# Kernel optimization log

Hardware: AMD Instinct MI355X
Metric: run time of the kernel (lower is better)

Reference implementation:

```python
import jax, jax.numpy as jnp
import numpy as np

B, N, K = 32, 2048, 16          # graphs, nodes per graph, knn neighbors
F_IN, F_OUT, P = 32, 64, 3      # feature dims, pos dim


def setup_inputs() -> dict:
    key = jax.random.key(0)
    ks = jax.random.split(key, 6)
    x = jax.random.normal(ks[0], (B * N, F_IN), dtype=jnp.float32)
    pos = jax.random.normal(ks[1], (B * N, P), dtype=jnp.float32)
    # contiguous equal-size graphs: batch[i] = i // N
    batch = (jnp.arange(B * N, dtype=jnp.int32) // N).astype(jnp.int32)
    W_edge = jax.random.normal(ks[2], (2 * F_IN, F_OUT), dtype=jnp.float32) * 0.1
    b_edge = jax.random.normal(ks[3], (F_OUT,), dtype=jnp.float32) * 0.1
    W_nn = jax.random.normal(ks[4], (F_IN, F_OUT), dtype=jnp.float32) * 0.1
    b_nn = jax.random.normal(ks[5], (F_OUT,), dtype=jnp.float32) * 0.1
    return {"x": x, "pos": pos, "W_edge": W_edge, "b_edge": b_edge,
            "W_nn": W_nn, "b_nn": b_nn, "batch": batch}


def reference(x, pos, W_edge, b_edge, W_nn, b_nn, batch):
    # batch is contiguous with N nodes per graph -> reshape to [B, N, .]
    xb = x.reshape(B, N, F_IN)
    pb = pos.reshape(B, N, P)

    # --- knn_graph on pos, per graph (flow='source_to_target') ---
    sq = jnp.sum(pb * pb, axis=-1)                                   # [B, N]
    d2 = sq[:, :, None] + sq[:, None, :] - 2.0 * jnp.einsum('bnd,bmd->bnm', pb, pb)
    d2 = d2 + jnp.eye(N, dtype=d2.dtype) * 1e30                      # exclude self-loops
    _, idx = jax.lax.top_k(-d2, K)                                   # idx[b, i, k] = k-th nearest j of i

    # --- EdgeConv: message = edge_nn(concat(x_i, x_j - x_i)), aggr=max at i ---
    x_j = jnp.take_along_axis(xb, idx.reshape(B, N * K, 1), axis=1).reshape(B, N, K, F_IN)
    x_i = xb[:, :, None, :]                                          # [B, N, 1, F_IN]
    msg = jnp.concatenate([jnp.broadcast_to(x_i, (B, N, K, F_IN)), x_j - x_i], axis=-1)
    h = jax.nn.relu(msg @ W_edge + b_edge)                           # [B, N, K, F_OUT]
    edge_out = jnp.max(h, axis=2)                                    # max-aggregate over neighbors

    # --- skip branch: nn(x) ---
    skip = jax.nn.relu(xb @ W_nn + b_nn)                             # [B, N, F_OUT]

    return (edge_out + skip).reshape(B * N, F_OUT)
```

## Files before the change

kernel.cpp:

```cpp
#include <hip/hip_runtime.h>

#define NB     32
#define NPTS   2048
#define KNN    16
#define FIN    32
#define FOUT   64

typedef __attribute__((ext_vector_type(8))) short bf16x8;
typedef __attribute__((ext_vector_type(4))) float f32x4;

__device__ inline unsigned bf16pk(float lo, float hi) {
    unsigned a = __float_as_uint(lo), b = __float_as_uint(hi);
    a = (a + 0x7fffu + ((a >> 16) & 1u)) >> 16;
    b = (b + 0x7fffu + ((b >> 16) & 1u)) >> 16;
    return (a & 0xffffu) | (b << 16);
}


#define CEA(x, y) { float _t = fminf(x, y); y = fmaxf(x, y); x = _t; }
#define CED(x, y) { float _t = fmaxf(x, y); y = fminf(x, y); x = _t; }

#define BMERGE16(dk) \
    CEA(dk[0],dk[8])  CEA(dk[1],dk[9])  CEA(dk[2],dk[10]) CEA(dk[3],dk[11]) \
    CEA(dk[4],dk[12]) CEA(dk[5],dk[13]) CEA(dk[6],dk[14]) CEA(dk[7],dk[15]) \
    CEA(dk[0],dk[4])  CEA(dk[1],dk[5])  CEA(dk[2],dk[6])  CEA(dk[3],dk[7])  \
    CEA(dk[8],dk[12]) CEA(dk[9],dk[13]) CEA(dk[10],dk[14]) CEA(dk[11],dk[15]) \
    CEA(dk[0],dk[2])  CEA(dk[1],dk[3])  CEA(dk[4],dk[6])  CEA(dk[5],dk[7])  \
    CEA(dk[8],dk[10]) CEA(dk[9],dk[11]) CEA(dk[12],dk[14]) CEA(dk[13],dk[15]) \
    CEA(dk[0],dk[1])  CEA(dk[2],dk[3])  CEA(dk[4],dk[5])  CEA(dk[6],dk[7])  \
    CEA(dk[8],dk[9])  CEA(dk[10],dk[11]) CEA(dk[12],dk[13]) CEA(dk[14],dk[15])

#define NET8(a) \
    CED(a[0],a[1]) CED(a[2],a[3]) CED(a[4],a[5]) CED(a[6],a[7]) \
    CED(a[0],a[2]) CED(a[1],a[3]) CED(a[4],a[6]) CED(a[5],a[7]) \
    CED(a[1],a[2]) CED(a[5],a[6]) \
    CED(a[0],a[4]) CED(a[1],a[5]) CED(a[2],a[6]) CED(a[3],a[7]) \
    CED(a[2],a[4]) CED(a[3],a[5]) \
    CED(a[1],a[2]) CED(a[3],a[4]) CED(a[5],a[6])

__global__ __launch_bounds__(256) void sq_kernel(
    const float* __restrict__ pos, float4* __restrict__ P4)
{
    const int i = blockIdx.x * 256 + threadIdx.x;
    const float px = pos[i*3 + 0];
    const float py = pos[i*3 + 1];
    const float pz = pos[i*3 + 2];
    const float sq = __fadd_rn(__fadd_rn(__fmul_rn(px,px), __fmul_rn(py,py)),
                               __fmul_rn(pz,pz));
    P4[i] = make_float4(px, py, pz, sq);
}

#define CH   8
#define CHL  (NPTS / CH)

#define D2P(C, DST)                                                        \
    {                                                                      \
        float _dot = __fmaf_rn(me.z, (C).z,                                \
                      __fmaf_rn(me.y, (C).y, __fmul_rn(me.x, (C).x)));     \
        DST = __fmaf_rn(-2.0f, _dot, (C).w);                               \
    }

#define SBATCH2(JB, EXCLF)                                                 \
    {                                                                      \
        float a[8], a2[8];                                                 \
        _Pragma("unroll")                                                  \
        for (int i = 0; i < 8; ++i) {                                      \
            const int j = (JB) + i;                                        \
            const float4 c = pb4[j];                                       \
            float d2;                                                      \
            D2P(c, d2)                                                     \
            a[i] = (EXCLF && j == q) ? 1e30f : d2;                         \
        }                                                                  \
        _Pragma("unroll")                                                  \
        for (int i = 0; i < 8; ++i) {                                      \
            const int j = (JB) + 8 + i;                                    \
            const float4 c = pb4[j];                                       \
            float d2;                                                      \
            D2P(c, d2)                                                     \
            a2[i] = (EXCLF && j == q) ? 1e30f : d2;                        \
        }                                                                  \
        NET8(a)                                                            \
        NET8(a2)                                                           \
        _Pragma("unroll")                                                  \
        for (int i = 0; i < 8; ++i) dk[8+i] = fminf(dk[8+i], a[i]);        \
        BMERGE16(dk)                                                       \
        _Pragma("unroll")                                                  \
        for (int i = 0; i < 8; ++i) dk[8+i] = fminf(dk[8+i], a2[i]);       \
        BMERGE16(dk)                                                       \
    }

#define APP(DD, JJ)                                                        \
    if ((DD) <= tthr) {                                                    \
        if ((DD) < tthr) {                                                 \
            if (cntS + cntT >= KNN) --cntT;                                \
            JL[base + cntS * 64 + l] = (JJ);                               \
            ++cntS;                                                        \
        } else if (cntS + cntT < KNN) {                                    \
            JL[base + (KNN - 1 - cntT) * 64 + l] = (JJ);                   \
            ++cntT;                                                        \
        }                                                                  \
    }

#define RESC(JJ, EXCLF)                                                    \
    {                                                                      \
        const float4 c = pb4[(JJ)];                                        \
        float d2;                                                          \
        D2P(c, d2)                                                         \
        if (EXCLF && (JJ) == q) d2 = 1e30f;                                \
        APP(d2, (JJ))                                                      \
    }

#define ESTRIDE 66

__global__ __launch_bounds__(512, 8) void knn_mlp_kernel(
    const float4* __restrict__ P4, const float* __restrict__ x,
    const float* __restrict__ W_edge, const float* __restrict__ b_edge,
    const float* __restrict__ W_nn,   const float* __restrict__ b_nn,
    float* __restrict__ out)
{
    __shared__ __attribute__((aligned(16))) char smem[38912];
    float* V    = (float*)smem;
    int*   CNTS = (int*)(smem + 32768);
    int*   IDX  = (int*)(smem + 34816);

    const int b    = blockIdx.x >> 5;
    const int slab = blockIdx.x & 31;
    const int t    = threadIdx.x;
    const int w    = __builtin_amdgcn_readfirstlane(t >> 6);
    const int l    = t & 63;

    {
        const float4* __restrict__ pb4 = P4 + (size_t)b * NPTS;

        const int    q  = slab * 64 + l;
        const float4 me = pb4[q];

        float dk[KNN];
        #pragma unroll
        for (int s = 0; s < KNN; ++s) dk[s] = 1e30f;

        const int j0  = w * CHL;
        const int exw = slab >> 2;
        const int lo  = j0 + (slab & 3) * 64;

        if (w == exw) {
            for (int jb = j0;      jb < lo;        jb += 16) SBATCH2(jb, false)
            for (int jb = lo;      jb < lo + 64;   jb += 16) SBATCH2(jb, true)
            for (int jb = lo + 64; jb < j0 + CHL;  jb += 16) SBATCH2(jb, false)
        } else {
            for (int jb = j0;      jb < j0 + CHL;  jb += 16) SBATCH2(jb, false)
        }

        #pragma unroll
        for (int s = 0; s < KNN; ++s)
            V[(w * KNN + s) * 64 + l] = dk[s];
        __syncthreads();

        for (int c2 = 0; c2 < CH; ++c2) {
            if (c2 == w) continue;
            float v[KNN];
            #pragma unroll
            for (int s2 = 0; s2 < KNN; ++s2)
                v[s2] = V[(c2 * KNN + s2) * 64 + l];
            #pragma unroll
            for (int s = 0; s < KNN; ++s) dk[s] = fminf(dk[s], v[KNN-1-s]);
            BMERGE16(dk)
        }
        const float tthr = dk[KNN-1];
        __syncthreads();

        int* JL = (int*)V;
        const int base = w * KNN * 64;
        int cntS = 0, cntT = 0;
        if (w == exw) {
            for (int j = j0;      j < lo;        ++j) RESC(j, false)
            for (int j = lo;      j < lo + 64;   ++j) RESC(j, true)
            for (int j = lo + 64; j < j0 + CHL;  ++j) RESC(j, false)
        } else {
            for (int j = j0;      j < j0 + CHL;  ++j) RESC(j, false)
        }
        CNTS[w * 64 + l] = cntS | (cntT << 16);
        __syncthreads();

        if (w == 0) {
            int outc = 0;
            for (int c2 = 0; c2 < CH; ++c2) {
                int cs = CNTS[c2 * 64 + l] & 0xffff;
                for (int s2 = 0; s2 < cs && outc < KNN; ++s2)
                    IDX[l * KNN + outc++] = JL[(c2 * KNN + s2) * 64 + l];
            }
            for (int c2 = 0; c2 < CH && outc < KNN; ++c2) {
                int ct = CNTS[c2 * 64 + l] >> 16;
                for (int s2 = 0; s2 < ct && outc < KNN; ++s2)
                    IDX[l * KNN + outc++] =
                        JL[(c2 * KNN + (KNN - 1 - s2)) * 64 + l];
            }
        }
        __syncthreads();
    }

    const int c15 = l & 15;
    const int g   = l >> 4;
    const int nbase = b * NPTS + slab * 64;
    const int gbase = b * NPTS;

    float* E = (float*)smem;
    float* S = (float*)(smem + 16896);

    const f32x4 zf = {0.f, 0.f, 0.f, 0.f};

    {
        const int ng = w & 3;
        const int f0 = (w >> 2) * 2;

        const float* rp = x + (size_t)(nbase + ng * 16 + c15) * FIN + g * 8;
        float4 v0 = *(const float4*)rp;
        float4 v1 = *(const float4*)(rp + 4);
        int4 pk = make_int4(bf16pk(v0.x, v0.y), bf16pk(v0.z, v0.w),
                            bf16pk(v1.x, v1.y), bf16pk(v1.z, v1.w));
        bf16x8 afi = *(bf16x8*)&pk;

        #pragma unroll
        for (int ff = 0; ff < 2; ++ff) {
            const int col = 16 * (f0 + ff) + c15;
            unsigned pd[4], pn[4];
            #pragma unroll
            for (int d = 0; d < 4; ++d) {
                const int k0 = g * 8 + 2 * d;
                float h0 = W_edge[(FIN + k0)     * FOUT + col];
                float h1 = W_edge[(FIN + k0 + 1) * FOUT + col];
                pd[d] = bf16pk(W_edge[k0       * FOUT + col] - h0,
                               W_edge[(k0 + 1) * FOUT + col] - h1);
                pn[d] = bf16pk(W_nn[k0 * FOUT + col], W_nn[(k0+1) * FOUT + col]);
            }
            int4 bd = make_int4(pd[0], pd[1], pd[2], pd[3]);
            int4 bn = make_int4(pn[0], pn[1], pn[2], pn[3]);
            f32x4 baseF = __builtin_amdgcn_mfma_f32_16x16x32_bf16(
                afi, *(bf16x8*)&bd, zf, 0, 0, 0);
            f32x4 skipF = __builtin_amdgcn_mfma_f32_16x16x32_bf16(
                afi, *(bf16x8*)&bn, zf, 0, 0, 0);
            const float be  = b_edge[col];
            const float bnn = b_nn[col];
            #pragma unroll
            for (int reg = 0; reg < 4; ++reg) {
                const int nd = ng * 16 + g * 4 + reg;
                E[nd * ESTRIDE + col] = baseF[reg] + be;
                S[nd * ESTRIDE + col] = fmaxf(skipF[reg] + bnn, 0.f);
            }
        }
    }
    __syncthreads();

    {
        const int n0l = w * 8;

        int4 Bhi[4];
        #pragma unroll
        for (int ff = 0; ff < 4; ++ff) {
            const int col = 16 * ff + c15;
            unsigned ph[4];
            #pragma unroll
            for (int d = 0; d < 4; ++d) {
                const int k0 = g * 8 + 2 * d;
                ph[d] = bf16pk(W_edge[(FIN + k0)     * FOUT + col],
                               W_edge[(FIN + k0 + 1) * FOUT + col]);
            }
            Bhi[ff] = make_int4(ph[0], ph[1], ph[2], ph[3]);
        }

        int nb0 = IDX[n0l * KNN + c15];
        const float* rpp = x + (size_t)(gbase + nb0) * FIN + g * 8;
        float4 pv0 = *(const float4*)rpp;
        float4 pv1 = *(const float4*)(rpp + 4);

        #pragma unroll 1
        for (int i = 0; i < 8; ++i) {
            float4 c0 = pv0, c1 = pv1;
            if (i < 7) {
                int nb = IDX[(n0l + i + 1) * KNN + c15];
                const float* rp2 = x + (size_t)(gbase + nb) * FIN + g * 8;
                pv0 = *(const float4*)rp2;
                pv1 = *(const float4*)(rp2 + 4);
            }
            int4 pk2 = make_int4(bf16pk(c0.x, c0.y), bf16pk(c0.z, c0.w),
                                 bf16pk(c1.x, c1.y), bf16pk(c1.z, c1.w));
            bf16x8 af = *(bf16x8*)&pk2;

            float rmax[4];
            #pragma unroll
            for (int ff = 0; ff < 4; ++ff) {
                f32x4 z = __builtin_amdgcn_mfma_f32_16x16x32_bf16(
                    af, *(bf16x8*)&Bhi[ff], zf, 0, 0, 0);
                float m = fmaxf(fmaxf(z[0], z[1]), fmaxf(z[2], z[3]));
                m = fmaxf(m, __shfl_xor(m, 16));
                m = fmaxf(m, __shfl_xor(m, 32));
                rmax[ff] = m;
            }
            float val = (g == 0) ? rmax[0] : (g == 1) ? rmax[1]
                      : (g == 2) ? rmax[2] : rmax[3];
            const int nd = n0l + i;
            float e = fmaxf(val + E[nd * ESTRIDE + g * 16 + c15], 0.f);
            float s = S[nd * ESTRIDE + g * 16 + c15];
            out[(size_t)(nbase + nd) * FOUT + g * 16 + c15] = e + s;
        }
    }
}

extern "C" void kernel_launch(void* const* d_in, const int* in_sizes, int n_in,
                              void* d_out, int out_size, void* d_ws, size_t ws_size,
                              hipStream_t stream) {
    const float* x      = (const float*)d_in[0];
    const float* pos    = (const float*)d_in[1];
    const float* W_edge = (const float*)d_in[2];
    const float* b_edge = (const float*)d_in[3];
    const float* W_nn   = (const float*)d_in[4];
    const float* b_nn   = (const float*)d_in[5];

    float4* P4   = (float4*)d_ws;
    float*  outp = (float*)d_out;

    sq_kernel     <<<NB * NPTS / 256, 256, 0, stream>>>(pos, P4);
    knn_mlp_kernel<<<NB * 32,         512, 0, stream>>>(P4, x, W_edge, b_edge,
                                                        W_nn, b_nn, outp);
}
```

Baseline: 204.7 us.

## Stage graph positions in LDS, pad IDX stride, double-buffer neighbor gathers

Each block now copies its graph's 2048 float4 positions into shared memory once and reads candidates from LDS in the distance scan, replacing repeated global or L1 loads. An extra barrier is added before the V buffer, which aliases P, is overwritten. The IDX row stride is padded to 17 to reduce LDS bank conflicts. The MFMA edge loop now prefetches two neighbor rows ahead to hide gather latency. LDS grows slightly, which may affect occupancy.

```diff
diff --git a/kernel.cpp b/kernel.cpp
--- a/kernel.cpp
+++ b/kernel.cpp
@@ -66,7 +66,7 @@
         _Pragma("unroll")                                                  \
         for (int i = 0; i < 8; ++i) {                                      \
             const int j = (JB) + i;                                        \
-            const float4 c = pb4[j];                                       \
+            const float4 c = P[j];                                         \
             float d2;                                                      \
             D2P(c, d2)                                                     \
             a[i] = (EXCLF && j == q) ? 1e30f : d2;                         \
@@ -74,7 +74,7 @@
         _Pragma("unroll")                                                  \
         for (int i = 0; i < 8; ++i) {                                      \
             const int j = (JB) + 8 + i;                                    \
-            const float4 c = pb4[j];                                       \
+            const float4 c = P[j];                                         \
             float d2;                                                      \
             D2P(c, d2)                                                     \
             a2[i] = (EXCLF && j == q) ? 1e30f : d2;                        \
@@ -111,6 +111,7 @@
     }
 
 #define ESTRIDE 66
+#define IDXS    17
 
 __global__ __launch_bounds__(512, 8) void knn_mlp_kernel(
     const float4* __restrict__ P4, const float* __restrict__ x,
@@ -118,10 +119,11 @@
     const float* __restrict__ W_nn,   const float* __restrict__ b_nn,
     float* __restrict__ out)
 {
-    __shared__ __attribute__((aligned(16))) char smem[38912];
-    float* V    = (float*)smem;
-    int*   CNTS = (int*)(smem + 32768);
-    int*   IDX  = (int*)(smem + 34816);
+    __shared__ __attribute__((aligned(16))) char smem[39168];
+    float4* P    = (float4*)smem;
+    float*  V    = (float*)smem;
+    int*    CNTS = (int*)(smem + 32768);
+    int*    IDX  = (int*)(smem + 34816);
 
     const int b    = blockIdx.x >> 5;
     const int slab = blockIdx.x & 31;
@@ -129,12 +131,19 @@
     const int w    = __builtin_amdgcn_readfirstlane(t >> 6);
     const int l    = t & 63;
 
+    const float4* __restrict__ pb4 = P4 + (size_t)b * NPTS;
+    const int q = slab * 64 + l;
+
+    #pragma unroll
+    for (int r = 0; r < 4; ++r) {
+        const int j = r * 512 + t;
+        P[j] = pb4[j];
+    }
+    __syncthreads();
+
+    const float4 me = P[q];
+
     {
-        const float4* __restrict__ pb4 = P4 + (size_t)b * NPTS;
-
-        const int    q  = slab * 64 + l;
-        const float4 me = pb4[q];
-
         float dk[KNN];
         #pragma unroll
         for (int s = 0; s < KNN; ++s) dk[s] = 1e30f;
@@ -150,6 +159,8 @@
         } else {
             for (int jb = j0;      jb < j0 + CHL;  jb += 16) SBATCH2(jb, false)
         }
+
+        __syncthreads();
 
         #pragma unroll
         for (int s = 0; s < KNN; ++s)
@@ -187,12 +198,12 @@
             for (int c2 = 0; c2 < CH; ++c2) {
                 int cs = CNTS[c2 * 64 + l] & 0xffff;
                 for (int s2 = 0; s2 < cs && outc < KNN; ++s2)
-                    IDX[l * KNN + outc++] = JL[(c2 * KNN + s2) * 64 + l];
+                    IDX[l * IDXS + outc++] = JL[(c2 * KNN + s2) * 64 + l];
             }
             for (int c2 = 0; c2 < CH && outc < KNN; ++c2) {
                 int ct = CNTS[c2 * 64 + l] >> 16;
                 for (int s2 = 0; s2 < ct && outc < KNN; ++s2)
-                    IDX[l * KNN + outc++] =
+                    IDX[l * IDXS + outc++] =
                         JL[(c2 * KNN + (KNN - 1 - s2)) * 64 + l];
             }
         }
@@ -268,40 +279,72 @@
             Bhi[ff] = make_int4(ph[0], ph[1], ph[2], ph[3]);
         }
 
-        int nb0 = IDX[n0l * KNN + c15];
-        const float* rpp = x + (size_t)(gbase + nb0) * FIN + g * 8;
-        float4 pv0 = *(const float4*)rpp;
-        float4 pv1 = *(const float4*)(rpp + 4);
+        int nbA = IDX[(n0l + 0) * IDXS + c15];
+        int nbB = IDX[(n0l + 1) * IDXS + c15];
+        const float* rpA = x + (size_t)(gbase + nbA) * FIN + g * 8;
+        const float* rpB = x + (size_t)(gbase + nbB) * FIN + g * 8;
+        float4 Aa = *(const float4*)rpA, Ab = *(const float4*)(rpA + 4);
+        float4 Ba = *(const float4*)rpB, Bb = *(const float4*)(rpB + 4);
 
         #pragma unroll 1
-        for (int i = 0; i < 8; ++i) {
-            float4 c0 = pv0, c1 = pv1;
-            if (i < 7) {
-                int nb = IDX[(n0l + i + 1) * KNN + c15];
+        for (int i = 0; i < 8; i += 2) {
+            float4 c0 = Aa, c1 = Ab;
+            if (i + 2 < 8) {
+                int nb = IDX[(n0l + i + 2) * IDXS + c15];
                 const float* rp2 = x + (size_t)(gbase + nb) * FIN + g * 8;
-                pv0 = *(const float4*)rp2;
-                pv1 = *(const float4*)(rp2 + 4);
-            }
-            int4 pk2 = make_int4(bf16pk(c0.x, c0.y), bf16pk(c0.z, c0.w),
-                                 bf16pk(c1.x, c1.y), bf16pk(c1.z, c1.w));
-            bf16x8 af = *(bf16x8*)&pk2;
-
-            float rmax[4];
-            #pragma unroll
-            for (int ff = 0; ff < 4; ++ff) {
-                f32x4 z = __builtin_amdgcn_mfma_f32_16x16x32_bf16(
-                    af, *(bf16x8*)&Bhi[ff], zf, 0, 0, 0);
-                float m = fmaxf(fmaxf(z[0], z[1]), fmaxf(z[2], z[3]));
-                m = fmaxf(m, __shfl_xor(m, 16));
-                m = fmaxf(m, __shfl_xor(m, 32));
-                rmax[ff] = m;
-            }
-            float val = (g == 0) ? rmax[0] : (g == 1) ? rmax[1]
-                      : (g == 2) ? rmax[2] : rmax[3];
-            const int nd = n0l + i;
-            float e = fmaxf(val + E[nd * ESTRIDE + g * 16 + c15], 0.f);
-            float s = S[nd * ESTRIDE + g * 16 + c15];
-            out[(size_t)(nbase + nd) * FOUT + g * 16 + c15] = e + s;
+                Aa = *(const float4*)rp2;
+                Ab = *(const float4*)(rp2 + 4);
+            }
+            {
+                int4 pk2 = make_int4(bf16pk(c0.x, c0.y), bf16pk(c0.z, c0.w),
+                                     bf16pk(c1.x, c1.y), bf16pk(c1.z, c1.w));
+                bf16x8 af = *(bf16x8*)&pk2;
+                float rmax[4];
+                #pragma unroll
+                for (int ff = 0; ff < 4; ++ff) {
+                    f32x4 z = __builtin_amdgcn_mfma_f32_16x16x32_bf16(
+                        af, *(bf16x8*)&Bhi[ff], zf, 0, 0, 0);
+                    float m = fmaxf(fmaxf(z[0], z[1]), fmaxf(z[2], z[3]));
+                    m = fmaxf(m, __shfl_xor(m, 16));
+                    m = fmaxf(m, __shfl_xor(m, 32));
+                    rmax[ff] = m;
+                }
+                float val = (g == 0) ? rmax[0] : (g == 1) ? rmax[1]
+                          : (g == 2) ? rmax[2] : rmax[3];
+                const int nd = n0l + i;
+                float e = fmaxf(val + E[nd * ESTRIDE + g * 16 + c15], 0.f);
+                float s = S[nd * ESTRIDE + g * 16 + c15];
+                out[(size_t)(nbase + nd) * FOUT + g * 16 + c15] = e + s;
+            }
+
+            float4 d0 = Ba, d1 = Bb;
+            if (i + 3 < 8) {
+                int nb = IDX[(n0l + i + 3) * IDXS + c15];
+                const float* rp2 = x + (size_t)(gbase + nb) * FIN + g * 8;
+                Ba = *(const float4*)rp2;
+                Bb = *(const float4*)(rp2 + 4);
+            }
+            {
+                int4 pk2 = make_int4(bf16pk(d0.x, d0.y), bf16pk(d0.z, d0.w),
+                                     bf16pk(d1.x, d1.y), bf16pk(d1.z, d1.w));
+                bf16x8 af = *(bf16x8*)&pk2;
+                float rmax[4];
+                #pragma unroll
+                for (int ff = 0; ff < 4; ++ff) {
+                    f32x4 z = __builtin_amdgcn_mfma_f32_16x16x32_bf16(
+                        af, *(bf16x8*)&Bhi[ff], zf, 0, 0, 0);
+                    float m = fmaxf(fmaxf(z[0], z[1]), fmaxf(z[2], z[3]));
+                    m = fmaxf(m, __shfl_xor(m, 16));
+                    m = fmaxf(m, __shfl_xor(m, 32));
+                    rmax[ff] = m;
+                }
+                float val = (g == 0) ? rmax[0] : (g == 1) ? rmax[1]
+                          : (g == 2) ? rmax[2] : rmax[3];
+                const int nd = n0l + i + 1;
+                float e = fmaxf(val + E[nd * ESTRIDE + g * 16 + c15], 0.f);
+                float s = S[nd * ESTRIDE + g * 16 + c15];
+                out[(size_t)(nbase + nd) * FOUT + g * 16 + c15] = e + s;
+            }
         }
     }
 }
```

After: 204.3 us. Within noise of the previous version (-0.2%).
